# Kernel optimization log

Hardware: AMD Instinct MI355X
Metric: run time of the kernel (lower is better)

Reference implementation:

```python
import jax, jax.numpy as jnp
import numpy as np

B, T, IN, H, O = 128, 512, 512, 512, 128

def setup_inputs() -> dict:
    key = jax.random.key(0)
    ks = jax.random.split(key, 16)
    s = 1.0 / np.sqrt(H)
    u = lambda k, shape: jax.random.uniform(k, shape, jnp.float32, -s, s)
    return {
        "x": jax.random.normal(ks[0], (B, T, IN), jnp.float32),
        # PyTorch GRU layer 0: weight_ih_l0 [3H, IN] (gate order r,z,n)
        "W_ih0": u(ks[1], (3 * H, IN)), "W_hh0": u(ks[2], (3 * H, H)),
        "b_ih0": u(ks[3], (3 * H,)),   "b_hh0": u(ks[4], (3 * H,)),
        # layer 1
        "W_ih1": u(ks[5], (3 * H, H)), "W_hh1": u(ks[6], (3 * H, H)),
        "b_ih1": u(ks[7], (3 * H,)),   "b_hh1": u(ks[8], (3 * H,)),
        # fc: Linear(H, O); fc_cate: Linear(O, 3O)
        "W_fc": u(ks[9], (O, H)),      "b_fc": u(ks[10], (O,)),
        "W_fcc": jax.random.uniform(ks[11], (3 * O, O), jnp.float32, -1/np.sqrt(O), 1/np.sqrt(O)),
        "b_fcc": jax.random.uniform(ks[12], (3 * O,), jnp.float32, -1/np.sqrt(O), 1/np.sqrt(O)),
    }

def _gru_layer(x, W_ih, W_hh, b_ih, b_hh):
    # x: [B, T, D] -> hidden sequence [B, T, H]. PyTorch gate order: r, z, n.
    Bm, Tm, _ = x.shape
    Hm = W_hh.shape[1]
    # precompute input projections for all timesteps: [B, T, 3H]
    xg = jnp.einsum('btd,gd->btg', x, W_ih) + b_ih
    b_hr, b_hz, b_hn = jnp.split(b_hh, 3)
    def step(h, xg_t):
        hg = h @ W_hh.T                       # [B, 3H]
        xr, xz, xn = jnp.split(xg_t, 3, axis=-1)
        hr, hz, hn = jnp.split(hg, 3, axis=-1)
        r = jax.nn.sigmoid(xr + hr + b_hr)
        z = jax.nn.sigmoid(xz + hz + b_hz)
        n = jnp.tanh(xn + r * (hn + b_hn))
        h_new = (1.0 - z) * n + z * h
        return h_new, h_new
    h0 = jnp.zeros((Bm, Hm), x.dtype)
    _, hs = jax.lax.scan(step, h0, jnp.swapaxes(xg, 0, 1))  # [T, B, H]
    return jnp.swapaxes(hs, 0, 1)

def reference(x, W_ih0, W_hh0, b_ih0, b_hh0, W_ih1, W_hh1, b_ih1, b_hh1, W_fc, b_fc, W_fcc, b_fcc):
    h1 = _gru_layer(x, W_ih0, W_hh0, b_ih0, b_hh0)   # layer 0 (dropout=0.0)
    h2 = _gru_layer(h1, W_ih1, W_hh1, b_ih1, b_hh1)  # layer 1
    out = h2[:, -1] @ W_fc.T + b_fc                  # [B, O]
    out_cate = out @ W_fcc.T + b_fcc                 # [B, 3O]
    return out[:, None, :], out_cate.reshape(-1, O, 3)
```

## Files before the change

kernel.cpp:

```cpp
#include <hip/hip_runtime.h>

#define Tn 512
#define Hn 512
#define HS 65536
#define NBLK 256

typedef __attribute__((ext_vector_type(8))) short s8v;
typedef __attribute__((ext_vector_type(4))) float f4v;
typedef __attribute__((ext_vector_type(4))) unsigned u4v;
typedef unsigned long long ull;

__device__ __forceinline__ unsigned short f2bf(float f) {
  unsigned u = __float_as_uint(f);
  u = u + 0x7fffu + ((u >> 16) & 1u);
  return (unsigned short)(u >> 16);
}
__device__ __forceinline__ float bf2f(unsigned short s) {
  return __uint_as_float(((unsigned)s) << 16);
}
__device__ __forceinline__ float sigm(float v) { return 1.f / (1.f + __expf(-v)); }
__device__ __forceinline__ float tanh_f(float v) {
  v = fminf(fmaxf(v, -15.f), 15.f);
  float e = __expf(2.f * v);
  return (e - 1.f) / (e + 1.f);
}
__device__ __forceinline__ f4v mfma3(s8v ah, s8v al, s8v whh, s8v wll, f4v c) {
  c = __builtin_amdgcn_mfma_f32_16x16x32_bf16(ah, whh, c, 0, 0, 0);
  c = __builtin_amdgcn_mfma_f32_16x16x32_bf16(al, whh, c, 0, 0, 0);
  c = __builtin_amdgcn_mfma_f32_16x16x32_bf16(ah, wll, c, 0, 0, 0);
  return c;
}

__device__ __forceinline__ ull ld_mall64(const ull* p) {
  return __hip_atomic_load(p, __ATOMIC_RELAXED, __HIP_MEMORY_SCOPE_AGENT);
}
__device__ __forceinline__ void st_mall(unsigned* p, unsigned v) {
  __hip_atomic_store(p, v, __ATOMIC_RELAXED, __HIP_MEMORY_SCOPE_AGENT);
}

__global__ void __launch_bounds__(512) __attribute__((amdgpu_waves_per_eu(2, 2)))
gru_fused(
    const float* __restrict__ x,
    const float* __restrict__ Wih0, const float* __restrict__ Whh0,
    const float* __restrict__ bih0, const float* __restrict__ bhh0,
    const float* __restrict__ Wih1, const float* __restrict__ Whh1,
    const float* __restrict__ bih1, const float* __restrict__ bhh1,
    int* __restrict__ flags,
    unsigned* __restrict__ h1ring,
    unsigned* __restrict__ h2ring,
    float* __restrict__ h2fin) {
  __shared__ __align__(16) float smem[38912];
  float (*part)[64][28] = (float (*)[64][28])smem;

  const int tid = threadIdx.x, lane = tid & 63, wv = tid >> 6;
  const bool inside = (wv < 4);
  const int kq = wv & 3;
  const bool comb = (wv == 4);
  const int colr = lane & 15, kg = lane >> 4;

  const int bid = blockIdx.x;
  const int g = bid & 7;
  const int layer = g & 1;
  const int mq = g >> 1;
  const int jg = bid >> 3;
  const int col = jg * 16 + colr;

  s8v* const wlf = (s8v*)((char*)smem + 57344 + wv * 12288);

  const float* W = inside ? (layer ? Wih1 : Wih0) : (layer ? Whh1 : Whh0);
  s8v wh[3][4];
#pragma unroll
  for (int gg = 0; gg < 3; ++gg) {
    const float* wrow = W + (size_t)(gg * Hn + col) * Hn + kq * 128 + kg * 8;
#pragma unroll
    for (int ks = 0; ks < 4; ++ks) {
      s8v lov;
#pragma unroll
      for (int e = 0; e < 8; ++e) {
        float v = wrow[ks * 32 + e];
        unsigned short hi = f2bf(v);
        wh[gg][ks][e] = (short)hi;
        lov[e] = (short)f2bf(v - bf2f(hi));
      }
      wlf[(gg * 4 + ks) * 64 + lane] = lov;
    }
  }

  float brz = 0, bzz = 0, bin = 0, bhn = 0;
  if (comb) {
    const float* bi = layer ? bih1 : bih0;
    const float* bb = layer ? bhh1 : bhh0;
    brz = bi[col] + bb[col];
    bzz = bi[Hn + col] + bb[Hn + col];
    bin = bi[2 * Hn + col];
    bhn = bb[2 * Hn + col];
  }

  const bool is_xw = (layer == 0 && inside);

  float4 xp[2][4][2];
  if (is_xw) {
#pragma unroll
    for (int mt = 0; mt < 2; ++mt) {
      const int rowA = mq * 32 + mt * 16 + colr;
      const float* xq = x + ((size_t)rowA * Tn) * 512 + kq * 128 + kg * 8;
#pragma unroll
      for (int ks = 0; ks < 4; ++ks) {
        xp[mt][ks][0] = *(const float4*)(xq + ks * 32);
        xp[mt][ks][1] = *(const float4*)(xq + ks * 32 + 4);
      }
    }
  }

  int* const ownline = flags + g * 32;
  int* const peerline = flags + (g ^ 1) * 32;

  float hown[2][4] = {{0.f, 0.f, 0.f, 0.f}, {0.f, 0.f, 0.f, 0.f}};

  __syncthreads();

#pragma unroll 1
  for (int t = 0; t < Tn; ++t) {
    if (wv == 0) {
      const int ta = t;
      const int tb = layer ? (t + 1) : (t - 3);
      const int* p = (lane < 32) ? (ownline + lane) : (peerline + (lane - 32));
      const int tgt = (lane < 32) ? ta : tb;
      for (;;) {
        int v = __hip_atomic_load(p, __ATOMIC_RELAXED, __HIP_MEMORY_SCOPE_AGENT);
        if (__all(v >= tgt)) break;
        __builtin_amdgcn_s_sleep(1);
      }
      asm volatile("" ::: "memory");
    }
    __syncthreads();

    f4v acc[2][3];
#pragma unroll
    for (int mt = 0; mt < 2; ++mt)
#pragma unroll
      for (int gg = 0; gg < 3; ++gg) acc[mt][gg] = (f4v){0.f, 0.f, 0.f, 0.f};

    if (is_xw) {
#pragma unroll
      for (int ks = 0; ks < 4; ++ks) {
        s8v wl0 = wlf[(0 * 4 + ks) * 64 + lane];
        s8v wl1 = wlf[(1 * 4 + ks) * 64 + lane];
        s8v wl2 = wlf[(2 * 4 + ks) * 64 + lane];
#pragma unroll
        for (int mt = 0; mt < 2; ++mt) {
          float v[8];
          v[0] = xp[mt][ks][0].x; v[1] = xp[mt][ks][0].y;
          v[2] = xp[mt][ks][0].z; v[3] = xp[mt][ks][0].w;
          v[4] = xp[mt][ks][1].x; v[5] = xp[mt][ks][1].y;
          v[6] = xp[mt][ks][1].z; v[7] = xp[mt][ks][1].w;
          u4v au, lu;
#pragma unroll
          for (int q = 0; q < 4; ++q) {
            unsigned u0 = __float_as_uint(v[2 * q]);
            unsigned u1 = __float_as_uint(v[2 * q + 1]);
            unsigned m0 = u0 & 0xffff0000u, m1 = u1 & 0xffff0000u;
            au[q] = (u0 >> 16) | m1;
            float l0 = v[2 * q] - __uint_as_float(m0);
            float l1 = v[2 * q + 1] - __uint_as_float(m1);
            lu[q] = (__float_as_uint(l0) >> 16) | (__float_as_uint(l1) & 0xffff0000u);
          }
          s8v ah = __builtin_bit_cast(s8v, au);
          s8v al = __builtin_bit_cast(s8v, lu);
          acc[mt][0] = mfma3(ah, al, wh[0][ks], wl0, acc[mt][0]);
          acc[mt][1] = mfma3(ah, al, wh[1][ks], wl1, acc[mt][1]);
          acc[mt][2] = mfma3(ah, al, wh[2][ks], wl2, acc[mt][2]);
        }
      }
#pragma unroll
      for (int mt = 0; mt < 2; ++mt)
#pragma unroll
        for (int gg = 0; gg < 3; ++gg)
          *(f4v*)&part[wv][lane][mt * 12 + gg * 4] = acc[mt][gg];
      const int tpre = (t + 1 < Tn) ? (t + 1) : (Tn - 1);
#pragma unroll
      for (int mt = 0; mt < 2; ++mt) {
        const int rowA = mq * 32 + mt * 16 + colr;
        const float* xq = x + ((size_t)rowA * Tn + tpre) * 512 + kq * 128 + kg * 8;
#pragma unroll
        for (int ks = 0; ks < 4; ++ks) {
          xp[mt][ks][0] = *(const float4*)(xq + ks * 32);
          xp[mt][ks][1] = *(const float4*)(xq + ks * 32 + 4);
        }
      }
    } else {
      const unsigned* src;
      if (inside)      src = h1ring + (size_t)(t & 3) * HS;
      else if (layer)  src = h2ring + (size_t)((t - 1) & 1) * HS;
      else             src = h1ring + (size_t)((t - 1) & 3) * HS;

      ull ub[2][16];
#pragma unroll
      for (int mt = 0; mt < 2; ++mt) {
        const int rowA = mq * 32 + mt * 16 + colr;
        const ull* pb64 = (const ull*)(src + (size_t)rowA * 512 + kq * 128 + kg * 8);
#pragma unroll
        for (int i = 0; i < 16; ++i)
          ub[mt][i] = ld_mall64(pb64 + (i >> 2) * 16 + (i & 3));
      }
#pragma unroll
      for (int ks = 0; ks < 4; ++ks) {
        s8v wl0 = wlf[(0 * 4 + ks) * 64 + lane];
        s8v wl1 = wlf[(1 * 4 + ks) * 64 + lane];
        s8v wl2 = wlf[(2 * 4 + ks) * 64 + lane];
#pragma unroll
        for (int mt = 0; mt < 2; ++mt) {
          u4v ahw, alw;
#pragma unroll
          for (int j = 0; j < 4; ++j) {
            unsigned a = (unsigned)ub[mt][ks * 4 + j];
            unsigned b = (unsigned)(ub[mt][ks * 4 + j] >> 32);
            ahw[j] = (a >> 16) | (b & 0xffff0000u);
            alw[j] = (a & 0xffffu) | (b << 16);
          }
          s8v AH = __builtin_bit_cast(s8v, ahw);
          s8v AL = __builtin_bit_cast(s8v, alw);
          acc[mt][0] = mfma3(AH, AL, wh[0][ks], wl0, acc[mt][0]);
          acc[mt][1] = mfma3(AH, AL, wh[1][ks], wl1, acc[mt][1]);
          acc[mt][2] = mfma3(AH, AL, wh[2][ks], wl2, acc[mt][2]);
        }
      }
      if (!comb) {
#pragma unroll
        for (int mt = 0; mt < 2; ++mt)
#pragma unroll
          for (int gg = 0; gg < 3; ++gg)
            *(f4v*)&part[wv][lane][mt * 12 + gg * 4] = acc[mt][gg];
      }
    }
    __syncthreads();

    if (comb) {
      unsigned* od = layer ? (h2ring + (size_t)(t & 1) * HS)
                           : (h1ring + (size_t)(t & 3) * HS);
#pragma unroll
      for (int mt = 0; mt < 2; ++mt) {
        const int moff = mt * 12;
        f4v xs[3], hsum[3];
#pragma unroll
        for (int gg = 0; gg < 3; ++gg) {
          xs[gg] = *(const f4v*)&part[0][lane][moff + gg * 4]
                 + *(const f4v*)&part[1][lane][moff + gg * 4]
                 + *(const f4v*)&part[2][lane][moff + gg * 4]
                 + *(const f4v*)&part[3][lane][moff + gg * 4];
          hsum[gg] = acc[mt][gg]
                   + *(const f4v*)&part[5][lane][moff + gg * 4]
                   + *(const f4v*)&part[6][lane][moff + gg * 4]
                   + *(const f4v*)&part[7][lane][moff + gg * 4];
        }
#pragma unroll
        for (int r = 0; r < 4; ++r) {
          float rr = sigm(xs[0][r] + hsum[0][r] + brz);
          float zz = sigm(xs[1][r] + hsum[1][r] + bzz);
          float nn = tanh_f(xs[2][r] + bin + rr * (hsum[2][r] + bhn));
          float h = (1.f - zz) * nn + zz * hown[mt][r];
          hown[mt][r] = h;
          const int row = mq * 32 + mt * 16 + kg * 4 + r;
          unsigned short hi = f2bf(h);
          unsigned pk = ((unsigned)hi << 16) | (unsigned)f2bf(h - bf2f(hi));
          st_mall(od + (size_t)row * 512 + col, pk);
          if (layer == 1 && t == Tn - 1) h2fin[(size_t)row * 512 + col] = h;
        }
      }
      asm volatile("s_waitcnt vmcnt(0)" ::: "memory");
      if (lane == 0)
        st_mall((unsigned*)(ownline + jg), (unsigned)(t + 1));
    }
  }
}

__global__ __launch_bounds__(256) void fc_kernel(const float* __restrict__ h2,
                                                 const float* __restrict__ Wfc,
                                                 const float* __restrict__ bfc,
                                                 float* __restrict__ out) {
  int gid = blockIdx.x * 256 + threadIdx.x;
  int b = gid >> 7, o = gid & 127;
  const float* hp = h2 + (size_t)b * Hn;
  const float* wp = Wfc + (size_t)o * Hn;
  float acc = bfc[o];
#pragma unroll 8
  for (int k = 0; k < Hn; k += 4) {
    float4 h = *(const float4*)(hp + k);
    float4 w = *(const float4*)(wp + k);
    acc = fmaf(h.x, w.x, acc); acc = fmaf(h.y, w.y, acc);
    acc = fmaf(h.z, w.z, acc); acc = fmaf(h.w, w.w, acc);
  }
  out[gid] = acc;
}

__global__ __launch_bounds__(256) void fcc_kernel(const float* __restrict__ outv,
                                                  const float* __restrict__ Wfcc,
                                                  const float* __restrict__ bfcc,
                                                  float* __restrict__ oc) {
  int gid = blockIdx.x * 256 + threadIdx.x;
  int b = gid / 384, g = gid - b * 384;
  const float* op = outv + (size_t)b * 128;
  const float* wp = Wfcc + (size_t)g * 128;
  float acc = bfcc[g];
#pragma unroll 8
  for (int k = 0; k < 128; k += 4) {
    float4 o4 = *(const float4*)(op + k);
    float4 w4 = *(const float4*)(wp + k);
    acc = fmaf(o4.x, w4.x, acc); acc = fmaf(o4.y, w4.y, acc);
    acc = fmaf(o4.z, w4.z, acc); acc = fmaf(o4.w, w4.w, acc);
  }
  oc[gid] = acc;
}

extern "C" void kernel_launch(void* const* d_in, const int* in_sizes, int n_in,
                              void* d_out, int out_size, void* d_ws, size_t ws_size,
                              hipStream_t stream) {
  (void)in_sizes; (void)n_in; (void)out_size; (void)ws_size;
  const float* x    = (const float*)d_in[0];
  const float* Wih0 = (const float*)d_in[1];
  const float* Whh0 = (const float*)d_in[2];
  const float* bih0 = (const float*)d_in[3];
  const float* bhh0 = (const float*)d_in[4];
  const float* Wih1 = (const float*)d_in[5];
  const float* Whh1 = (const float*)d_in[6];
  const float* bih1 = (const float*)d_in[7];
  const float* bhh1 = (const float*)d_in[8];
  const float* Wfc  = (const float*)d_in[9];
  const float* bfc  = (const float*)d_in[10];
  const float* Wfcc = (const float*)d_in[11];
  const float* bfcc = (const float*)d_in[12];

  char* w = (char*)d_ws;
  int* flags = (int*)w;
  unsigned* h1ring = (unsigned*)(w + 8192);
  unsigned* h2ring = h1ring + 4 * HS;
  float* h2fin = (float*)(h2ring + 2 * HS);
  const size_t total = 8192 + (size_t)4 * HS * 4 + (size_t)2 * HS * 4 + (size_t)HS * 4;

  hipMemsetAsync(d_ws, 0, total, stream);

  gru_fused<<<NBLK, 512, 0, stream>>>(x, Wih0, Whh0, bih0, bhh0,
                                      Wih1, Whh1, bih1, bhh1,
                                      flags, h1ring, h2ring, h2fin);

  float* out = (float*)d_out;
  fc_kernel<<<64, 256, 0, stream>>>(h2fin, Wfc, bfc, out);
  fcc_kernel<<<192, 256, 0, stream>>>(out, Wfcc, bfcc, out + 16384);
}
```

Measured before the change: 5.872 ms.

## Distribute flag polling per wave and split gate combine across two waves

```diff
diff --git a/kernel.cpp b/kernel.cpp
--- a/kernel.cpp
+++ b/kernel.cpp
@@ -38,7 +38,16 @@
   __hip_atomic_store(p, v, __ATOMIC_RELAXED, __HIP_MEMORY_SCOPE_AGENT);
 }
 
-__global__ void __launch_bounds__(512) __attribute__((amdgpu_waves_per_eu(2, 2)))
+__device__ __forceinline__ void poll_line(const int* p, int tgt) {
+  for (;;) {
+    int v = __hip_atomic_load(p, __ATOMIC_RELAXED, __HIP_MEMORY_SCOPE_AGENT);
+    if (__all(v >= tgt)) break;
+    __builtin_amdgcn_s_sleep(1);
+  }
+  asm volatile("" ::: "memory");
+}
+
+__global__ void __launch_bounds__(512, 2)
 gru_fused(
     const float* __restrict__ x,
     const float* __restrict__ Wih0, const float* __restrict__ Whh0,
@@ -55,7 +64,7 @@
   const int tid = threadIdx.x, lane = tid & 63, wv = tid >> 6;
   const bool inside = (wv < 4);
   const int kq = wv & 3;
-  const bool comb = (wv == 4);
+  const bool comb = (wv == 4 || wv == 5);
   const int colr = lane & 15, kg = lane >> 4;
 
   const int bid = blockIdx.x;
@@ -112,29 +121,16 @@
     }
   }
 
-  int* const ownline = flags + g * 32;
-  int* const peerline = flags + (g ^ 1) * 32;
-
-  float hown[2][4] = {{0.f, 0.f, 0.f, 0.f}, {0.f, 0.f, 0.f, 0.f}};
+  int* const ownline = flags + g * 64;
+  int* const peerline = flags + (g ^ 1) * 64;
+  const int pidx = ((lane >> 3) & 1) * 32 + kq * 8 + (lane & 7);
+
+  float hown[4] = {0.f, 0.f, 0.f, 0.f};
 
   __syncthreads();
 
 #pragma unroll 1
   for (int t = 0; t < Tn; ++t) {
-    if (wv == 0) {
-      const int ta = t;
-      const int tb = layer ? (t + 1) : (t - 3);
-      const int* p = (lane < 32) ? (ownline + lane) : (peerline + (lane - 32));
-      const int tgt = (lane < 32) ? ta : tb;
-      for (;;) {
-        int v = __hip_atomic_load(p, __ATOMIC_RELAXED, __HIP_MEMORY_SCOPE_AGENT);
-        if (__all(v >= tgt)) break;
-        __builtin_amdgcn_s_sleep(1);
-      }
-      asm volatile("" ::: "memory");
-    }
-    __syncthreads();
-
     f4v acc[2][3];
 #pragma unroll
     for (int mt = 0; mt < 2; ++mt)
@@ -190,9 +186,12 @@
       }
     } else {
       const unsigned* src;
-      if (inside)      src = h1ring + (size_t)(t & 3) * HS;
-      else if (layer)  src = h2ring + (size_t)((t - 1) & 1) * HS;
-      else             src = h1ring + (size_t)((t - 1) & 3) * HS;
+      if (inside)      { src = h1ring + (size_t)(t & 3) * HS;
+                         poll_line(peerline + pidx, t + 1); }
+      else if (layer)  { src = h2ring + (size_t)((t - 1) & 1) * HS;
+                         poll_line(ownline + pidx, t); }
+      else             { src = h1ring + (size_t)((t - 1) & 3) * HS;
+                         poll_line(ownline + pidx, t); }
 
       ull ub[2][16];
 #pragma unroll
@@ -225,7 +224,15 @@
           acc[mt][2] = mfma3(AH, AL, wh[2][ks], wl2, acc[mt][2]);
         }
       }
-      if (!comb) {
+      if (wv == 4) {
+#pragma unroll
+        for (int gg = 0; gg < 3; ++gg)
+          *(f4v*)&part[4][lane][gg * 4] = acc[1][gg];
+      } else if (wv == 5) {
+#pragma unroll
+        for (int gg = 0; gg < 3; ++gg)
+          *(f4v*)&part[5][lane][gg * 4] = acc[0][gg];
+      } else {
 #pragma unroll
         for (int mt = 0; mt < 2; ++mt)
 #pragma unroll
@@ -235,41 +242,45 @@
     }
     __syncthreads();
 
+    f4v xs[3], hsum[3];
     if (comb) {
+      const int mt = wv - 4;
+      const int moff = mt * 12;
+#pragma unroll
+      for (int gg = 0; gg < 3; ++gg) {
+        xs[gg] = *(const f4v*)&part[0][lane][moff + gg * 4]
+               + *(const f4v*)&part[1][lane][moff + gg * 4]
+               + *(const f4v*)&part[2][lane][moff + gg * 4]
+               + *(const f4v*)&part[3][lane][moff + gg * 4];
+        hsum[gg] = acc[mt][gg]
+                 + *(const f4v*)&part[wv == 4 ? 5 : 4][lane][gg * 4]
+                 + *(const f4v*)&part[6][lane][moff + gg * 4]
+                 + *(const f4v*)&part[7][lane][moff + gg * 4];
+      }
+    }
+    __syncthreads();
+
+    if (comb) {
+      const int mt = wv - 4;
+      if (layer == 0) poll_line(peerline + lane, t - 3);
       unsigned* od = layer ? (h2ring + (size_t)(t & 1) * HS)
                            : (h1ring + (size_t)(t & 3) * HS);
 #pragma unroll
-      for (int mt = 0; mt < 2; ++mt) {
-        const int moff = mt * 12;
-        f4v xs[3], hsum[3];
-#pragma unroll
-        for (int gg = 0; gg < 3; ++gg) {
-          xs[gg] = *(const f4v*)&part[0][lane][moff + gg * 4]
-                 + *(const f4v*)&part[1][lane][moff + gg * 4]
-                 + *(const f4v*)&part[2][lane][moff + gg * 4]
-                 + *(const f4v*)&part[3][lane][moff + gg * 4];
-          hsum[gg] = acc[mt][gg]
-                   + *(const f4v*)&part[5][lane][moff + gg * 4]
-                   + *(const f4v*)&part[6][lane][moff + gg * 4]
-                   + *(const f4v*)&part[7][lane][moff + gg * 4];
-        }
-#pragma unroll
-        for (int r = 0; r < 4; ++r) {
-          float rr = sigm(xs[0][r] + hsum[0][r] + brz);
-          float zz = sigm(xs[1][r] + hsum[1][r] + bzz);
-          float nn = tanh_f(xs[2][r] + bin + rr * (hsum[2][r] + bhn));
-          float h = (1.f - zz) * nn + zz * hown[mt][r];
-          hown[mt][r] = h;
-          const int row = mq * 32 + mt * 16 + kg * 4 + r;
-          unsigned short hi = f2bf(h);
-          unsigned pk = ((unsigned)hi << 16) | (unsigned)f2bf(h - bf2f(hi));
-          st_mall(od + (size_t)row * 512 + col, pk);
-          if (layer == 1 && t == Tn - 1) h2fin[(size_t)row * 512 + col] = h;
-        }
+      for (int r = 0; r < 4; ++r) {
+        float rr = sigm(xs[0][r] + hsum[0][r] + brz);
+        float zz = sigm(xs[1][r] + hsum[1][r] + bzz);
+        float nn = tanh_f(xs[2][r] + bin + rr * (hsum[2][r] + bhn));
+        float h = (1.f - zz) * nn + zz * hown[r];
+        hown[r] = h;
+        const int row = mq * 32 + mt * 16 + kg * 4 + r;
+        unsigned short hi = f2bf(h);
+        unsigned pk = ((unsigned)hi << 16) | (unsigned)f2bf(h - bf2f(hi));
+        st_mall(od + (size_t)row * 512 + col, pk);
+        if (layer == 1 && t == Tn - 1) h2fin[(size_t)row * 512 + col] = h;
       }
       asm volatile("s_waitcnt vmcnt(0)" ::: "memory");
       if (lane == 0)
-        st_mall((unsigned*)(ownline + jg), (unsigned)(t + 1));
+        st_mall((unsigned*)(ownline + mt * 32 + jg), (unsigned)(t + 1));
     }
   }
 }
```

Result: slower. 9.162 ms (+56.0%).
